# Kernel optimization log

Measured on AMD Instinct MI355X. Metric: run time of the kernel, lower is better.

## Reference

```python
import jax, jax.numpy as jnp
import numpy as np
import math

B, T, D_MODEL, N_HEADS = 2, 2048, 2048, 16
D_HEAD = D_MODEL // N_HEADS
ROPE_THETA = 10000.0


def setup_inputs() -> dict:
    key = jax.random.key(0)
    ks = jax.random.split(key, 4)
    x = jax.random.normal(ks[0], (B, T, D_MODEL), dtype=jnp.float32)
    # causal mask: True = masked (matches torch masked_fill semantics)
    mask = jnp.triu(jnp.ones((T, T), dtype=bool), k=1)[None, None]  # [1,1,T,T]
    # rotary freqs: complex freqs_cis = exp(i * t * theta^(-2j/d)) -> cos/sin parts
    inv_freq = 1.0 / (ROPE_THETA ** (jnp.arange(0, D_HEAD, 2, dtype=jnp.float32) / D_HEAD))
    angles = jnp.arange(T, dtype=jnp.float32)[:, None] * inv_freq[None, :]  # [T, D_HEAD//2]
    freqs_cos = jnp.cos(angles)
    freqs_sin = jnp.sin(angles)
    s = 1.0 / math.sqrt(D_MODEL)
    Wqkv = jax.random.normal(ks[1], (D_MODEL, 3 * D_MODEL), dtype=jnp.float32) * s
    bqkv = jnp.zeros((3 * D_MODEL,), dtype=jnp.float32)
    Wproj = jax.random.normal(ks[2], (D_MODEL, D_MODEL), dtype=jnp.float32) * s
    bproj = jnp.zeros((D_MODEL,), dtype=jnp.float32)
    return {"x": x, "mask": mask, "freqs_cos": freqs_cos, "freqs_sin": freqs_sin,
            "Wqkv": Wqkv, "bqkv": bqkv, "Wproj": Wproj, "bproj": bproj}


def _rope(t, cos, sin):
    # t: [B,H,T,D]; cos/sin: [1,1,T,D//2]. Complex multiply on (even, odd) pairs.
    t2 = t.reshape(*t.shape[:-1], -1, 2)
    t_re, t_im = t2[..., 0], t2[..., 1]
    out_re = t_re * cos - t_im * sin
    out_im = t_re * sin + t_im * cos
    return jnp.stack([out_re, out_im], axis=-1).reshape(t.shape)


def reference(x, mask, freqs_cos, freqs_sin, Wqkv, bqkv, Wproj, bproj):
    Bb, Tt, C = x.shape
    qkv = x @ Wqkv + bqkv                                   # [B,T,3C]
    q, k, v = jnp.split(qkv, 3, axis=-1)
    def heads(t):
        return t.reshape(Bb, Tt, N_HEADS, D_HEAD).transpose(0, 2, 1, 3)  # [B,H,T,D]
    q, k, v = heads(q), heads(k), heads(v)
    cos = freqs_cos[None, None]                              # [1,1,T,D//2]
    sin = freqs_sin[None, None]
    q = _rope(q, cos, sin)
    k = _rope(k, cos, sin)
    att = jnp.einsum('bhqd,bhkd->bhqk', q, k) / math.sqrt(D_HEAD)
    att = jnp.where(mask, -jnp.inf, att)
    att = jax.nn.softmax(att, axis=-1)
    # attn_dropout is identity in eval mode
    out = jnp.einsum('bhqk,bhkd->bhqd', att, v)              # [B,H,T,D]
    out = out.transpose(0, 2, 1, 3).reshape(Bb, Tt, C)
    return (out @ Wproj + bproj, k, v)
```

## Files before the change

kernel.cpp:

```cpp
#include <hip/hip_runtime.h>
#include <hip/hip_bf16.h>

#define T_SEQ 2048
#define DM    2048
#define NH    16
#define DH    128
#define NBH   32
#define MROWS 4096

typedef __bf16 bf16x8 __attribute__((ext_vector_type(8)));
typedef __bf16 bf16x4 __attribute__((ext_vector_type(4)));
typedef float  f32x4  __attribute__((ext_vector_type(4)));

#define MFMA16 __builtin_amdgcn_mfma_f32_16x16x32_bf16

__device__ __forceinline__ void async_copy16(const void* g, void* l) {
  __builtin_amdgcn_global_load_lds((const __attribute__((address_space(1))) void*)g,
                                   (__attribute__((address_space(3))) void*)l, 16, 0, 0);
}


__global__ void cast_bf16_k(const float* __restrict__ x, __bf16* __restrict__ xb) {
  int i = (blockIdx.x * 256 + threadIdx.x) * 4;
  float4 v = *reinterpret_cast<const float4*>(x + i);
  bf16x4 o;
  o[0] = (__bf16)v.x; o[1] = (__bf16)v.y; o[2] = (__bf16)v.z; o[3] = (__bf16)v.w;
  *reinterpret_cast<bf16x4*>(xb + i) = o;
}

__global__ void transpose_cast_w(const float* __restrict__ W, __bf16* __restrict__ WT,
                                 int K, int N) {
  __shared__ float tile[32][33];
  int n0 = blockIdx.x * 32, k0 = blockIdx.y * 32;
  int tx = threadIdx.x, ty = threadIdx.y;
  #pragma unroll
  for (int i = 0; i < 4; i++)
    tile[ty + i * 8][tx] = W[(size_t)(k0 + ty + i * 8) * N + n0 + tx];
  __syncthreads();
  #pragma unroll
  for (int i = 0; i < 4; i++)
    WT[(size_t)(n0 + ty + i * 8) * K + k0 + tx] = (__bf16)tile[tx][ty + i * 8];
}

__global__ void transpose_v(const __bf16* __restrict__ Vb, __bf16* __restrict__ Vtb) {
  __shared__ __bf16 tile[32][34];
  int t0 = blockIdx.x * 32, d0 = blockIdx.y * 32, bh = blockIdx.z;
  const __bf16* src = Vb + (size_t)bh * T_SEQ * DH;
  __bf16* dst = Vtb + (size_t)bh * DH * T_SEQ;
  int tx = threadIdx.x, ty = threadIdx.y;
  #pragma unroll
  for (int i = 0; i < 4; i++)
    tile[ty + i * 8][tx] = src[(size_t)(t0 + ty + i * 8) * DH + d0 + tx];
  __syncthreads();
  #pragma unroll
  for (int i = 0; i < 4; i++)
    dst[(size_t)(d0 + ty + i * 8) * T_SEQ + t0 + tx] = tile[tx][ty + i * 8];
}


__device__ __forceinline__ bf16x8 rds(const __bf16* base, int row, int chunk) {
  return *reinterpret_cast<const bf16x8*>(
      reinterpret_cast<const char*>(base) + row * 128 + ((chunk ^ (row & 7)) << 4));
}

__device__ __forceinline__ void stage64(const __bf16* g, int K, int kt, char* lds,
                                        int wave, int lane) {
  #pragma unroll
  for (int j = 0; j < 4; j++) {
    int r = wave * 32 + j * 8 + (lane >> 3);
    int c = lane & 7;
    const char* src = (const char*)g + (size_t)r * (K * 2) + kt * 128 + ((c ^ (r & 7)) << 4);
    async_copy16(src, lds + wave * 4096 + j * 1024);
  }
}

template <int EPI>
__global__ __launch_bounds__(256, 2) void gemm_bt(
    const __bf16* __restrict__ A, const __bf16* __restrict__ Bt, int K,
    const float* __restrict__ bias,
    const float* __restrict__ fcos, const float* __restrict__ fsin,
    __bf16* __restrict__ Qb, __bf16* __restrict__ Kb, __bf16* __restrict__ Vb,
    float* __restrict__ kout, float* __restrict__ vout,
    float* __restrict__ outp) {
  __shared__ __align__(16) char smem[65536];
  const int tid = threadIdx.x, lane = tid & 63, wave = tid >> 6;
  const int hi = lane >> 4, lo = lane & 15;
  const int wm = (wave >> 1) * 64, wn = (wave & 1) * 64;
  const __bf16* Ab = A + (size_t)blockIdx.y * 128 * K;
  const __bf16* Bb = Bt + (size_t)blockIdx.x * 128 * K;
  f32x4 acc[4][4] = {};
  const int NK = K >> 6;

  stage64(Ab, K, 0, smem, wave, lane);
  stage64(Bb, K, 0, smem + 32768, wave, lane);
  __syncthreads();

  for (int t = 0; t < NK; ++t) {
    const int sel = (t & 1) ? 16384 : 0;
    const __bf16* Ac = (const __bf16*)(smem + sel);
    const __bf16* Bc = (const __bf16*)(smem + 32768 + sel);
    if (t + 1 < NK) {
      stage64(Ab, K, t + 1, smem + (sel ^ 16384), wave, lane);
      stage64(Bb, K, t + 1, smem + 32768 + (sel ^ 16384), wave, lane);
    }
    bf16x8 a0[4], b0[4], a1[4], b1[4];
    #pragma unroll
    for (int m = 0; m < 4; ++m) a0[m] = rds(Ac, wm + m * 16 + lo, hi);
    #pragma unroll
    for (int n = 0; n < 4; ++n) b0[n] = rds(Bc, wn + n * 16 + lo, hi);
    __builtin_amdgcn_s_setprio(1);
    #pragma unroll
    for (int m = 0; m < 4; ++m)
      #pragma unroll
      for (int n = 0; n < 4; ++n)
        acc[m][n] = MFMA16(a0[m], b0[n], acc[m][n], 0, 0, 0);
    __builtin_amdgcn_s_setprio(0);
    #pragma unroll
    for (int m = 0; m < 4; ++m) a1[m] = rds(Ac, wm + m * 16 + lo, 4 + hi);
    #pragma unroll
    for (int n = 0; n < 4; ++n) b1[n] = rds(Bc, wn + n * 16 + lo, 4 + hi);
    __builtin_amdgcn_s_setprio(1);
    #pragma unroll
    for (int m = 0; m < 4; ++m)
      #pragma unroll
      for (int n = 0; n < 4; ++n)
        acc[m][n] = MFMA16(a1[m], b1[n], acc[m][n], 0, 0, 0);
    __builtin_amdgcn_s_setprio(0);
    __syncthreads();
  }

  float* sc = (float*)smem;
  const int rl_r = tid >> 3;
  const int cb   = (tid & 7) * 16;
  #pragma unroll
  for (int cc = 0; cc < 4; ++cc) {
    __syncthreads();
    if ((wave >> 1) == (cc >> 1)) {
      #pragma unroll
      for (int mm = 0; mm < 2; ++mm) {
        int m = (cc & 1) * 2 + mm;
        #pragma unroll
        for (int j = 0; j < 4; ++j) {
          int col = wn + j * 16 + lo;
          int rl = mm * 16 + hi * 4;
          #pragma unroll
          for (int r = 0; r < 4; ++r)
            sc[(rl + r) * 132 + col] = acc[m][j][r];
        }
      }
    }
    __syncthreads();
    float v[16];
    #pragma unroll
    for (int q = 0; q < 4; ++q)
      *reinterpret_cast<float4*>(&v[q * 4]) =
          *reinterpret_cast<const float4*>(&sc[rl_r * 132 + cb + q * 4]);
    const int row = blockIdx.y * 128 + cc * 32 + rl_r;
    const int n0  = blockIdx.x * 128 + cb;
    #pragma unroll
    for (int q = 0; q < 4; ++q) {
      float4 bv = *reinterpret_cast<const float4*>(&bias[n0 + q * 4]);
      v[q * 4 + 0] += bv.x; v[q * 4 + 1] += bv.y;
      v[q * 4 + 2] += bv.z; v[q * 4 + 3] += bv.w;
    }
    if (EPI == 1) {
      const int which = n0 >> 11;
      const int wn2 = n0 & 2047, h = wn2 >> 7, d0 = wn2 & 127;
      const int b = row >> 11, tt = row & 2047;
      if (which < 2) {
        const float* cp = fcos + tt * 64 + (d0 >> 1);
        const float* sp = fsin + tt * 64 + (d0 >> 1);
        float4 c0 = *reinterpret_cast<const float4*>(cp);
        float4 c1 = *reinterpret_cast<const float4*>(cp + 4);
        float4 s0 = *reinterpret_cast<const float4*>(sp);
        float4 s1 = *reinterpret_cast<const float4*>(sp + 4);
        float cs[8] = {c0.x, c0.y, c0.z, c0.w, c1.x, c1.y, c1.z, c1.w};
        float sn[8] = {s0.x, s0.y, s0.z, s0.w, s1.x, s1.y, s1.z, s1.w};
        #pragma unroll
        for (int p = 0; p < 8; ++p) {
          float re = v[2 * p], im = v[2 * p + 1];
          v[2 * p]     = re * cs[p] - im * sn[p];
          v[2 * p + 1] = re * sn[p] + im * cs[p];
        }
      }
      size_t base = (((size_t)(b * NH + h)) * T_SEQ + tt) * DH + d0;
      bf16x8 o0, o1;
      #pragma unroll
      for (int p = 0; p < 8; ++p) { o0[p] = (__bf16)v[p]; o1[p] = (__bf16)v[8 + p]; }
      if (which == 0) {
        *reinterpret_cast<bf16x8*>(Qb + base) = o0;
        *reinterpret_cast<bf16x8*>(Qb + base + 8) = o1;
      } else if (which == 1) {
        *reinterpret_cast<bf16x8*>(Kb + base) = o0;
        *reinterpret_cast<bf16x8*>(Kb + base + 8) = o1;
        #pragma unroll
        for (int q = 0; q < 4; ++q)
          *reinterpret_cast<float4*>(kout + base + q * 4) =
              *reinterpret_cast<const float4*>(&v[q * 4]);
      } else {
        *reinterpret_cast<bf16x8*>(Vb + base) = o0;
        *reinterpret_cast<bf16x8*>(Vb + base + 8) = o1;
        #pragma unroll
        for (int q = 0; q < 4; ++q)
          *reinterpret_cast<float4*>(vout + base + q * 4) =
              *reinterpret_cast<const float4*>(&v[q * 4]);
      }
    } else {
      float* op = outp + (size_t)row * DM + n0;
      #pragma unroll
      for (int q = 0; q < 4; ++q)
        *reinterpret_cast<float4*>(op + q * 4) =
            *reinterpret_cast<const float4*>(&v[q * 4]);
    }
  }
}


__device__ __forceinline__ bf16x8 lds_frag(const __bf16* base, int row, int chunk) {
  return *reinterpret_cast<const bf16x8*>(
      reinterpret_cast<const char*>(base) + row * 256 + ((chunk ^ (row & 7)) << 4));
}

__device__ __forceinline__ void ldK(const __bf16* Kg, int kt, int wave, int lane,
                                    bf16x8 k[4]) {
  const char* g = (const char*)(Kg + (size_t)kt * 64 * DH);
  #pragma unroll
  for (int j = 0; j < 4; j++) {
    int off = j * 4096 + wave * 1024;
    int r = (off >> 8) + (lane >> 4);
    int c = lane & 15;
    k[j] = *reinterpret_cast<const bf16x8*>(g + (size_t)r * 256 + ((c ^ (r & 7)) << 4));
  }
}

__device__ __forceinline__ void ldV(const __bf16* Vg, int kt, int wave, int lane,
                                    bf16x8 v[4]) {
  const char* g = (const char*)Vg;
  const int colB = kt * 128;
  #pragma unroll
  for (int j = 0; j < 4; j++) {
    int off = j * 4096 + wave * 1024;
    int r = (off >> 7) + (lane >> 3);
    int c = lane & 7;
    v[j] = *reinterpret_cast<const bf16x8*>(g + (size_t)r * (T_SEQ * 2) + colB + ((c ^ (r & 7)) << 4));
  }
}

__device__ __forceinline__ void commitKV(__bf16* Ks, __bf16* Vts, int wave, int lane,
                                         const bf16x8 k[4], const bf16x8 v[4]) {
  #pragma unroll
  for (int j = 0; j < 4; j++)
    *reinterpret_cast<bf16x8*>((char*)Ks + j * 4096 + wave * 1024 + lane * 16) = k[j];
  #pragma unroll
  for (int j = 0; j < 4; j++)
    *reinterpret_cast<bf16x8*>((char*)Vts + j * 4096 + wave * 1024 + lane * 16) = v[j];
}

__global__ __launch_bounds__(256, 2) void attn_fwd(
    const __bf16* __restrict__ Qb, const __bf16* __restrict__ Kb,
    const __bf16* __restrict__ Vtb, __bf16* __restrict__ att_out) {
  __shared__ __bf16 Ks[64 * 128];
  __shared__ __bf16 Vts[128 * 64];
  __shared__ __bf16 Ps[4 * 16 * 64];
  const int tid = threadIdx.x, lane = tid & 63, wave = tid >> 6;
  const int hi = lane >> 4, lo = lane & 15;
  const int linear = (int)blockIdx.x;
  const int xcd = linear & 7, rest = linear >> 3;
  const int bh = xcd + 8 * (rest >> 4);
  const int pair = rest & 15;
  const int b = bh >> 4, h = bh & 15;
  const __bf16* Qg = Qb + (size_t)bh * T_SEQ * DH;
  const __bf16* Kg = Kb + (size_t)bh * T_SEQ * DH;
  const __bf16* Vg = Vtb + (size_t)bh * DH * T_SEQ;
  const float scale = 0.08838834764831845f;
  const float L2E = 1.4426950408889634f;
  __bf16* Pw = Ps + wave * 1024;

  for (int pass = 0; pass < 2; ++pass) {
    const int qj = pass ? (31 - pair) : pair;
    const int q0 = qj * 64;
    const int qg = q0 + wave * 16 + lo;
    bf16x8 qf[4];
    const __bf16* qp = Qg + (size_t)qg * DH + hi * 8;
    #pragma unroll
    for (int ks = 0; ks < 4; ++ks) qf[ks] = *reinterpret_cast<const bf16x8*>(qp + ks * 32);
    f32x4 oacc[8] = {};
    float m = -3e38f, l = 0.f;
    const int NT = qj + 1;

    bf16x8 kst[4], vst[4];
    ldK(Kg, 0, wave, lane, kst);
    ldV(Vg, 0, wave, lane, vst);

    for (int kt = 0; kt < NT; ++kt) {
      __syncthreads();
      commitKV(Ks, Vts, wave, lane, kst, vst);
      __syncthreads();
      if (kt + 1 < NT) {
        ldK(Kg, kt + 1, wave, lane, kst);
        ldV(Vg, kt + 1, wave, lane, vst);
      }

      f32x4 sacc[4] = {};
      __builtin_amdgcn_s_setprio(1);
      #pragma unroll
      for (int ks = 0; ks < 4; ++ks)
        #pragma unroll
        for (int sf = 0; sf < 4; ++sf) {
          bf16x8 ak = lds_frag(Ks, sf * 16 + lo, ks * 4 + hi);
          sacc[sf] = MFMA16(ak, qf[ks], sacc[sf], 0, 0, 0);
        }
      __builtin_amdgcn_s_setprio(0);
      const bool diag = (kt == NT - 1);
      float mx = -3e38f;
      #pragma unroll
      for (int sf = 0; sf < 4; ++sf)
        #pragma unroll
        for (int r = 0; r < 4; ++r) {
          float v = sacc[sf][r] * scale;
          if (diag && (kt * 64 + sf * 16 + hi * 4 + r) > qg) v = -3e38f;
          sacc[sf][r] = v;
          mx = fmaxf(mx, v);
        }
      mx = fmaxf(mx, __shfl_xor(mx, 16, 64));
      mx = fmaxf(mx, __shfl_xor(mx, 32, 64));
      const bool nr = __all(mx - m <= 8.0f);
      if (!nr) {
        float mnew = fmaxf(m, mx);
        float alpha = __builtin_exp2f((m - mnew) * L2E);
        m = mnew;
        l *= alpha;
        #pragma unroll
        for (int df = 0; df < 8; ++df) {
          oacc[df][0] *= alpha; oacc[df][1] *= alpha;
          oacc[df][2] *= alpha; oacc[df][3] *= alpha;
        }
      }
      float rs = 0.f;
      #pragma unroll
      for (int sf = 0; sf < 4; ++sf)
        #pragma unroll
        for (int r = 0; r < 4; ++r) {
          float p = __builtin_exp2f((sacc[sf][r] - m) * L2E);
          sacc[sf][r] = p;
          rs += p;
        }
      rs += __shfl_xor(rs, 16, 64);
      rs += __shfl_xor(rs, 32, 64);
      l += rs;
      #pragma unroll
      for (int sf = 0; sf < 4; ++sf) {
        bf16x4 pk;
        pk[0] = (__bf16)sacc[sf][0]; pk[1] = (__bf16)sacc[sf][1];
        pk[2] = (__bf16)sacc[sf][2]; pk[3] = (__bf16)sacc[sf][3];
        int byte = sf * 32 + hi * 8;
        int chunk = byte >> 4, rem = byte & 15;
        char* p = (char*)Pw + lo * 128 + (((chunk ^ (lo & 7)) << 4) | rem);
        *reinterpret_cast<bf16x4*>(p) = pk;
      }
      __builtin_amdgcn_s_setprio(1);
      #pragma unroll
      for (int ks = 0; ks < 2; ++ks) {
        bf16x8 bp = rds(Pw, lo, ks * 4 + hi);
        #pragma unroll
        for (int df = 0; df < 8; ++df) {
          bf16x8 av = rds(Vts, df * 16 + lo, ks * 4 + hi);
          oacc[df] = MFMA16(av, bp, oacc[df], 0, 0, 0);
        }
      }
      __builtin_amdgcn_s_setprio(0);
    }

    float inv = 1.0f / l;
    int qrow = b * T_SEQ + q0 + wave * 16 + lo;
    #pragma unroll
    for (int df = 0; df < 8; ++df) {
      bf16x4 pk;
      pk[0] = (__bf16)(oacc[df][0] * inv);
      pk[1] = (__bf16)(oacc[df][1] * inv);
      pk[2] = (__bf16)(oacc[df][2] * inv);
      pk[3] = (__bf16)(oacc[df][3] * inv);
      int d = df * 16 + hi * 4;
      *reinterpret_cast<bf16x4*>(att_out + (size_t)qrow * DM + h * DH + d) = pk;
    }
  }
}


extern "C" void kernel_launch(void* const* d_in, const int* in_sizes, int n_in,
                              void* d_out, int out_size, void* d_ws, size_t ws_size,
                              hipStream_t stream) {
  const float* x     = (const float*)d_in[0];
  const float* fcos  = (const float*)d_in[2];
  const float* fsin  = (const float*)d_in[3];
  const float* Wqkv  = (const float*)d_in[4];
  const float* bqkv  = (const float*)d_in[5];
  const float* Wproj = (const float*)d_in[6];
  const float* bproj = (const float*)d_in[7];
  float* out  = (float*)d_out;
  float* kout = out + (size_t)8388608;
  float* vout = out + (size_t)16777216;

  char* ws = (char*)d_ws;
  __bf16* xb     = (__bf16*)(ws);
  __bf16* WqkvT  = (__bf16*)(ws + 16777216);
  __bf16* WprojT = (__bf16*)(ws + 41943040);
  __bf16* Qb     = (__bf16*)(ws + 50331648);
  __bf16* Kb     = (__bf16*)(ws + 67108864);
  __bf16* Vb     = (__bf16*)(ws + 83886080);
  __bf16* Vtb    = (__bf16*)(ws + 100663296);
  __bf16* att    = xb;

  cast_bf16_k<<<8192, 256, 0, stream>>>(x, xb);
  transpose_cast_w<<<dim3(192, 64), dim3(32, 8), 0, stream>>>(Wqkv, WqkvT, DM, 3 * DM);
  transpose_cast_w<<<dim3(64, 64), dim3(32, 8), 0, stream>>>(Wproj, WprojT, DM, DM);
  gemm_bt<1><<<dim3(48, 32), 256, 0, stream>>>(xb, WqkvT, DM, bqkv, fcos, fsin,
                                               Qb, Kb, Vb, kout, vout, nullptr);
  transpose_v<<<dim3(64, 4, NBH), dim3(32, 8), 0, stream>>>(Vb, Vtb);
  attn_fwd<<<512, 256, 0, stream>>>(Qb, Kb, Vtb, att);
  gemm_bt<0><<<dim3(16, 32), 256, 0, stream>>>(att, WprojT, DM, bproj, nullptr, nullptr,
                                               nullptr, nullptr, nullptr, nullptr, nullptr, out);
}
```

Before: 276.9 us.

## Load V fragments directly from global into registers, bypassing LDS

Removes the LDS staging buffer for the transposed V tile. Each wave now loads its own MFMA A-operand fragments for V straight from global memory into registers, prefetching the next tile after the PV matmul. This drops the V LDS writes and reads and halves the LDS footprint. In exchange, every wave fetches the whole V tile, so global/L2 traffic for V is four times higher. Those loads are less coalesced (64-byte runs per row), and holding 16 extra bf16x8 values per lane adds register pressure that may cause spills.

```diff
diff --git a/kernel.cpp b/kernel.cpp
--- a/kernel.cpp
+++ b/kernel.cpp
@@ -233,34 +233,27 @@
   }
 }
 
-__device__ __forceinline__ void ldV(const __bf16* Vg, int kt, int wave, int lane,
-                                    bf16x8 v[4]) {
-  const char* g = (const char*)Vg;
-  const int colB = kt * 128;
-  #pragma unroll
-  for (int j = 0; j < 4; j++) {
-    int off = j * 4096 + wave * 1024;
-    int r = (off >> 7) + (lane >> 3);
-    int c = lane & 7;
-    v[j] = *reinterpret_cast<const bf16x8*>(g + (size_t)r * (T_SEQ * 2) + colB + ((c ^ (r & 7)) << 4));
-  }
-}
-
-__device__ __forceinline__ void commitKV(__bf16* Ks, __bf16* Vts, int wave, int lane,
-                                         const bf16x8 k[4], const bf16x8 v[4]) {
+__device__ __forceinline__ void commitK(__bf16* Ks, int wave, int lane,
+                                        const bf16x8 k[4]) {
   #pragma unroll
   for (int j = 0; j < 4; j++)
     *reinterpret_cast<bf16x8*>((char*)Ks + j * 4096 + wave * 1024 + lane * 16) = k[j];
-  #pragma unroll
-  for (int j = 0; j < 4; j++)
-    *reinterpret_cast<bf16x8*>((char*)Vts + j * 4096 + wave * 1024 + lane * 16) = v[j];
+}
+
+__device__ __forceinline__ void ldV(const __bf16* Vg, int kt, int hi, int lo,
+                                    bf16x8 av[2][8]) {
+  #pragma unroll
+  for (int ks = 0; ks < 2; ++ks)
+    #pragma unroll
+    for (int df = 0; df < 8; ++df)
+      av[ks][df] = *reinterpret_cast<const bf16x8*>(
+          Vg + (size_t)(df * 16 + lo) * T_SEQ + kt * 64 + (ks * 4 + hi) * 8);
 }
 
 __global__ __launch_bounds__(256, 2) void attn_fwd(
     const __bf16* __restrict__ Qb, const __bf16* __restrict__ Kb,
     const __bf16* __restrict__ Vtb, __bf16* __restrict__ att_out) {
   __shared__ __bf16 Ks[64 * 128];
-  __shared__ __bf16 Vts[128 * 64];
   __shared__ __bf16 Ps[4 * 16 * 64];
   const int tid = threadIdx.x, lane = tid & 63, wave = tid >> 6;
   const int hi = lane >> 4, lo = lane & 15;
@@ -288,18 +281,17 @@
     float m = -3e38f, l = 0.f;
     const int NT = qj + 1;
 
-    bf16x8 kst[4], vst[4];
+    bf16x8 kst[4];
+    bf16x8 av[2][8];
     ldK(Kg, 0, wave, lane, kst);
-    ldV(Vg, 0, wave, lane, vst);
+    ldV(Vg, 0, hi, lo, av);
 
     for (int kt = 0; kt < NT; ++kt) {
       __syncthreads();
-      commitKV(Ks, Vts, wave, lane, kst, vst);
+      commitK(Ks, wave, lane, kst);
       __syncthreads();
-      if (kt + 1 < NT) {
+      if (kt + 1 < NT)
         ldK(Kg, kt + 1, wave, lane, kst);
-        ldV(Vg, kt + 1, wave, lane, vst);
-      }
 
       f32x4 sacc[4] = {};
       __builtin_amdgcn_s_setprio(1);
@@ -363,12 +355,12 @@
       for (int ks = 0; ks < 2; ++ks) {
         bf16x8 bp = rds(Pw, lo, ks * 4 + hi);
         #pragma unroll
-        for (int df = 0; df < 8; ++df) {
-          bf16x8 av = rds(Vts, df * 16 + lo, ks * 4 + hi);
-          oacc[df] = MFMA16(av, bp, oacc[df], 0, 0, 0);
-        }
+        for (int df = 0; df < 8; ++df)
+          oacc[df] = MFMA16(av[ks][df], bp, oacc[df], 0, 0, 0);
       }
       __builtin_amdgcn_s_setprio(0);
+      if (kt + 1 < NT)
+        ldV(Vg, kt + 1, hi, lo, av);
     }
 
     float inv = 1.0f / l;
```

New measurement: 357.3 us. 1.29x slower.
